# Kernel tuning notes

Hardware: AMD Instinct MI355X
Metric: run time of the kernel (lower is better)

Reference implementation:

```python
import jax, jax.numpy as jnp
import numpy as np

N, T, V, F = 16, 128, 64, 16


def setup_inputs() -> dict:
    key = jax.random.key(0)
    k1, k2 = jax.random.split(key)
    x = jax.random.normal(k1, (N, T, V, F), dtype=jnp.float32)
    a_spatial = jax.random.normal(k2, (F, 1), dtype=jnp.float32) * 0.05
    return {"x": x, "a_spatial": a_spatial}


def reference(x, a_spatial):
    # x: [N, T, V, F]; pairwise abs-diff across vertices -> [N, T, V, V, F]
    diff = jnp.abs(x[:, :, :, None, :] - x[:, :, None, :, :])
    # mean over time -> [N, V, V, F] (matches transpose([0,4,2,3,1]) + reduce_mean(axis=1))
    mean_diff = jnp.mean(diff, axis=1)
    # score: dot with a_Spatial [F,1] then squeeze -> [N, V, V]
    score = jnp.einsum('nijf,fo->nij', mean_diff, a_spatial)
    tmpS = jnp.exp(jax.nn.relu(score))
    # row-normalize over axis=1 (as in the original K.sum(..., axis=1))
    return tmpS / jnp.sum(tmpS, axis=1, keepdims=True)
```

## Files before the change

kernel.cpp:

```cpp
#include <hip/hip_runtime.h>
#include <hip/hip_bf16.h>
#include <math.h>


#define Nn 16
#define Tt 128
#define Vv 64
#define Ff 16
#define CHUNKS 32
#define TC 4
#define JSPLIT 4
#define JPW 4
#define PITCH 20

__global__ __launch_bounds__(256, 8) void gls_scores(const float* __restrict__ x,
                                                     const float* __restrict__ a,
                                                     float* __restrict__ ws) {
    __shared__ float xs[TC * Vv * PITCH];

    const int c   = blockIdx.x;
    const int n   = blockIdx.y;
    const int z   = blockIdx.z;
    const int tid = threadIdx.x;
    const int i   = tid & 63;
    const int w   = __builtin_amdgcn_readfirstlane(tid >> 6);
    const int j0  = z * (Vv / JSPLIT) + w * JPW;

    const float4* xg = (const float4*)(x + (size_t)(n * Tt + c * TC) * (Vv * Ff));
#pragma unroll
    for (int k = 0; k < 4; ++k) {
        const int f4  = tid + k * 256;
        const float4 val = xg[f4];
        const int p   = f4 << 2;
        const int tl  = p >> 10;
        const int rem = p & 1023;
        const int v   = rem >> 4;
        const int f   = rem & 15;
        *(float4*)&xs[(tl * Vv + v) * PITCH + f] = val;
    }

    float af[Ff];
#pragma unroll
    for (int f = 0; f < Ff; ++f) af[f] = a[f];

    __syncthreads();

    float acc[JPW] = {0.f, 0.f, 0.f, 0.f};

#pragma unroll
    for (int tt = 0; tt < TC; ++tt) {
        const float* xi = &xs[(tt * Vv + i) * PITCH];
        const float4 A0 = *(const float4*)(xi);
        const float4 A1 = *(const float4*)(xi + 4);
        const float4 A2 = *(const float4*)(xi + 8);
        const float4 A3 = *(const float4*)(xi + 12);
#pragma unroll
        for (int jj = 0; jj < JPW; ++jj) {
            const float* xj = &xs[(tt * Vv + j0 + jj) * PITCH];
            const float4 B0 = *(const float4*)(xj);
            const float4 B1 = *(const float4*)(xj + 4);
            const float4 B2 = *(const float4*)(xj + 8);
            const float4 B3 = *(const float4*)(xj + 12);
            float s = acc[jj];
            s = fmaf(fabsf(A0.x - B0.x), af[0],  s);
            s = fmaf(fabsf(A0.y - B0.y), af[1],  s);
            s = fmaf(fabsf(A0.z - B0.z), af[2],  s);
            s = fmaf(fabsf(A0.w - B0.w), af[3],  s);
            s = fmaf(fabsf(A1.x - B1.x), af[4],  s);
            s = fmaf(fabsf(A1.y - B1.y), af[5],  s);
            s = fmaf(fabsf(A1.z - B1.z), af[6],  s);
            s = fmaf(fabsf(A1.w - B1.w), af[7],  s);
            s = fmaf(fabsf(A2.x - B2.x), af[8],  s);
            s = fmaf(fabsf(A2.y - B2.y), af[9],  s);
            s = fmaf(fabsf(A2.z - B2.z), af[10], s);
            s = fmaf(fabsf(A2.w - B2.w), af[11], s);
            s = fmaf(fabsf(A3.x - B3.x), af[12], s);
            s = fmaf(fabsf(A3.y - B3.y), af[13], s);
            s = fmaf(fabsf(A3.z - B3.z), af[14], s);
            s = fmaf(fabsf(A3.w - B3.w), af[15], s);
            acc[jj] = s;
        }
    }

    float* wsb = ws + (((size_t)n * CHUNKS + c) * Vv + j0) * Vv;
#pragma unroll
    for (int jj = 0; jj < JPW; ++jj)
        wsb[jj * Vv + i] = acc[jj];
}

__global__ __launch_bounds__(256) void gls_norm(const float* __restrict__ ws,
                                                float* __restrict__ out) {
    const int n   = blockIdx.x;
    const int jq  = blockIdx.y;
    const int tid = threadIdx.x;
    const int i   = tid & 63;
    const int w   = tid >> 6;
    const int j   = jq * 4 + w;

    const float* wsn = ws + (size_t)n * CHUNKS * (Vv * Vv);
    float s = 0.f;
#pragma unroll
    for (int cc = 0; cc < CHUNKS; ++cc)
        s += wsn[(cc * Vv + j) * Vv + i];

    const float e = expf(fmaxf(s * (1.0f / (float)Tt), 0.0f));
    float tsum = e;
#pragma unroll
    for (int m = 1; m < 64; m <<= 1) tsum += __shfl_xor(tsum, m, 64);

    out[((size_t)n * Vv + i) * Vv + j] = e / tsum;
}

extern "C" void kernel_launch(void* const* d_in, const int* in_sizes, int n_in,
                              void* d_out, int out_size, void* d_ws, size_t ws_size,
                              hipStream_t stream) {
    const float* x = (const float*)d_in[0];
    const float* a = (const float*)d_in[1];
    float* out = (float*)d_out;
    float* ws  = (float*)d_ws;

    dim3 g1(CHUNKS, Nn, JSPLIT);
    gls_scores<<<g1, 256, 0, stream>>>(x, a, ws);
    dim3 g2(Nn, 16);
    gls_norm<<<g2, 256, 0, stream>>>(ws, out);
}
```

Measured before the change: 69.94 us.

## Fuse score and normalization kernels into one with in-block time reduction

```diff
diff --git a/kernel.cpp b/kernel.cpp
--- a/kernel.cpp
+++ b/kernel.cpp
@@ -1,5 +1,4 @@
 #include <hip/hip_runtime.h>
-#include <hip/hip_bf16.h>
 #include <math.h>
 
 
@@ -7,60 +6,42 @@
 #define Tt 128
 #define Vv 64
 #define Ff 16
-#define CHUNKS 32
-#define TC 4
-#define JSPLIT 4
-#define JPW 4
-#define PITCH 20
+#define TSPLIT 4
+#define TPW (Tt / TSPLIT)
+#define JPB 4
 
-__global__ __launch_bounds__(256, 8) void gls_scores(const float* __restrict__ x,
-                                                     const float* __restrict__ a,
-                                                     float* __restrict__ ws) {
-    __shared__ float xs[TC * Vv * PITCH];
-
-    const int c   = blockIdx.x;
-    const int n   = blockIdx.y;
-    const int z   = blockIdx.z;
+__global__ __launch_bounds__(256) void gls_fused(const float* __restrict__ x,
+                                                 const float* __restrict__ a,
+                                                 float* __restrict__ out) {
+    const int n   = blockIdx.x;
+    const int z   = blockIdx.y;
+    const int j0  = z * JPB;
     const int tid = threadIdx.x;
     const int i   = tid & 63;
     const int w   = __builtin_amdgcn_readfirstlane(tid >> 6);
-    const int j0  = z * (Vv / JSPLIT) + w * JPW;
-
-    const float4* xg = (const float4*)(x + (size_t)(n * Tt + c * TC) * (Vv * Ff));
-#pragma unroll
-    for (int k = 0; k < 4; ++k) {
-        const int f4  = tid + k * 256;
-        const float4 val = xg[f4];
-        const int p   = f4 << 2;
-        const int tl  = p >> 10;
-        const int rem = p & 1023;
-        const int v   = rem >> 4;
-        const int f   = rem & 15;
-        *(float4*)&xs[(tl * Vv + v) * PITCH + f] = val;
-    }
 
     float af[Ff];
 #pragma unroll
     for (int f = 0; f < Ff; ++f) af[f] = a[f];
 
-    __syncthreads();
+    float acc[JPB] = {0.f, 0.f, 0.f, 0.f};
 
-    float acc[JPW] = {0.f, 0.f, 0.f, 0.f};
+    const float4* xb = (const float4*)x + (size_t)(n * Tt + w * TPW) * (Vv * Ff / 4);
 
+#pragma unroll 2
+    for (int t = 0; t < TPW; ++t) {
+        const float4* xt = xb + (size_t)t * (Vv * Ff / 4);
+        const float4 A0 = xt[i * 4 + 0];
+        const float4 A1 = xt[i * 4 + 1];
+        const float4 A2 = xt[i * 4 + 2];
+        const float4 A3 = xt[i * 4 + 3];
 #pragma unroll
-    for (int tt = 0; tt < TC; ++tt) {
-        const float* xi = &xs[(tt * Vv + i) * PITCH];
-        const float4 A0 = *(const float4*)(xi);
-        const float4 A1 = *(const float4*)(xi + 4);
-        const float4 A2 = *(const float4*)(xi + 8);
-        const float4 A3 = *(const float4*)(xi + 12);
-#pragma unroll
-        for (int jj = 0; jj < JPW; ++jj) {
-            const float* xj = &xs[(tt * Vv + j0 + jj) * PITCH];
-            const float4 B0 = *(const float4*)(xj);
-            const float4 B1 = *(const float4*)(xj + 4);
-            const float4 B2 = *(const float4*)(xj + 8);
-            const float4 B3 = *(const float4*)(xj + 12);
+        for (int jj = 0; jj < JPB; ++jj) {
+            const float4* xj = xt + (j0 + jj) * 4;
+            const float4 B0 = xj[0];
+            const float4 B1 = xj[1];
+            const float4 B2 = xj[2];
+            const float4 B3 = xj[3];
             float s = acc[jj];
             s = fmaf(fabsf(A0.x - B0.x), af[0],  s);
             s = fmaf(fabsf(A0.y - B0.y), af[1],  s);
@@ -82,33 +63,19 @@
         }
     }
 
-    float* wsb = ws + (((size_t)n * CHUNKS + c) * Vv + j0) * Vv;
+    __shared__ float part[TSPLIT][JPB][Vv];
 #pragma unroll
-    for (int jj = 0; jj < JPW; ++jj)
-        wsb[jj * Vv + i] = acc[jj];
-}
+    for (int jj = 0; jj < JPB; ++jj)
+        part[w][jj][i] = acc[jj];
+    __syncthreads();
 
-__global__ __launch_bounds__(256) void gls_norm(const float* __restrict__ ws,
-                                                float* __restrict__ out) {
-    const int n   = blockIdx.x;
-    const int jq  = blockIdx.y;
-    const int tid = threadIdx.x;
-    const int i   = tid & 63;
-    const int w   = tid >> 6;
-    const int j   = jq * 4 + w;
-
-    const float* wsn = ws + (size_t)n * CHUNKS * (Vv * Vv);
-    float s = 0.f;
-#pragma unroll
-    for (int cc = 0; cc < CHUNKS; ++cc)
-        s += wsn[(cc * Vv + j) * Vv + i];
-
+    float s = part[0][w][i] + part[1][w][i] + part[2][w][i] + part[3][w][i];
     const float e = expf(fmaxf(s * (1.0f / (float)Tt), 0.0f));
     float tsum = e;
 #pragma unroll
     for (int m = 1; m < 64; m <<= 1) tsum += __shfl_xor(tsum, m, 64);
 
-    out[((size_t)n * Vv + i) * Vv + j] = e / tsum;
+    out[((size_t)n * Vv + i) * Vv + (j0 + w)] = e / tsum;
 }
 
 extern "C" void kernel_launch(void* const* d_in, const int* in_sizes, int n_in,
@@ -117,10 +84,8 @@
     const float* x = (const float*)d_in[0];
     const float* a = (const float*)d_in[1];
     float* out = (float*)d_out;
-    float* ws  = (float*)d_ws;
+    (void)d_ws; (void)ws_size;
 
-    dim3 g1(CHUNKS, Nn, JSPLIT);
-    gls_scores<<<g1, 256, 0, stream>>>(x, a, ws);
-    dim3 g2(Nn, 16);
-    gls_norm<<<g2, 256, 0, stream>>>(ws, out);
+    dim3 g(Nn, Vv / JPB);
+    gls_fused<<<g, 256, 0, stream>>>(x, a, out);
 }
```

Result: slower. 78.83 us (+12.7%).
